# Kernel optimization log

Hardware: AMD Instinct MI355X
Metric: run time of the kernel (lower is better)

Reference implementation:

```python
import jax, jax.numpy as jnp
import numpy as np

N = 50000      # nodes
E = 400000     # edges
D_IN = 128
D = 256        # d_hidden
H = 8          # heads
C = D // H     # head dim (PyG out_channels)
L = 3          # layers
SCALE = 1.0 / np.sqrt(C).astype(np.float32)


def setup_inputs() -> dict:
    key = jax.random.key(0)
    ks = jax.random.split(key, 16)
    w = lambda k, shape: (jax.random.normal(k, shape, jnp.float32) * 0.02)
    inp = {
        "x": jax.random.normal(ks[0], (N, D_IN), jnp.float32),
        "edge_index": jax.random.randint(ks[1], (2, E), 0, N, dtype=jnp.int64),
        # input projection
        "W_in": w(ks[2], (D, D_IN)), "b_in": jnp.zeros((D,), jnp.float32),
        # stacked TransformerConv params: query/key/value/skip linears per layer
        "Wq": w(ks[3], (L, D, D)), "bq": jnp.zeros((L, D), jnp.float32),
        "Wk": w(ks[4], (L, D, D)), "bk": jnp.zeros((L, D), jnp.float32),
        "Wv": w(ks[5], (L, D, D)), "bv": jnp.zeros((L, D), jnp.float32),
        "Ws": w(ks[6], (L, D, D)), "bs": jnp.zeros((L, D), jnp.float32),
        # layer norms
        "ln_g": jnp.ones((L, D), jnp.float32), "ln_b": jnp.zeros((L, D), jnp.float32),
        # edge classifier: Linear(2D,D) -> ReLU -> Linear(D,1)
        "Wec1": w(ks[7], (D, 2 * D)), "bec1": jnp.zeros((D,), jnp.float32),
        "Wec2": w(ks[8], (1, D)), "bec2": jnp.zeros((1,), jnp.float32),
        # param predictor: Linear(2D,D) -> ReLU -> Linear(D,2) -> softplus
        "Wpp1": w(ks[9], (D, 2 * D)), "bpp1": jnp.zeros((D,), jnp.float32),
        "Wpp2": w(ks[10], (2, D)), "bpp2": jnp.zeros((2,), jnp.float32),
    }
    return inp


def _layer_norm(h, g, b):
    mu = jnp.mean(h, axis=-1, keepdims=True)
    var = jnp.mean(jnp.square(h - mu), axis=-1, keepdims=True)
    return (h - mu) * jax.lax.rsqrt(var + 1e-5) * g + b


def _transformer_conv(h, src, dst, Wq, bq, Wk, bk, Wv, bv, Ws, bs):
    # PyG TransformerConv (concat=True, root_weight=True, eval mode / no dropout)
    q = (h @ Wq.T + bq).reshape(N, H, C)
    k = (h @ Wk.T + bk).reshape(N, H, C)
    v = (h @ Wv.T + bv).reshape(N, H, C)
    # per-edge attention logits: query at dst, key at src  -> [E, H]
    alpha = jnp.einsum('ehc,ehc->eh', q[dst], k[src]) * SCALE
    # scatter-softmax over incoming edges of each dst node
    amax = jax.lax.stop_gradient(jax.ops.segment_max(alpha, dst, num_segments=N))
    ea = jnp.exp(alpha - amax[dst])
    denom = jax.ops.segment_sum(ea, dst, num_segments=N)
    a = ea / (denom[dst] + 1e-16)
    # weighted scatter-add of values  -> [N, H, C] -> [N, D]
    out = jax.ops.segment_sum(a[:, :, None] * v[src], dst, num_segments=N).reshape(N, D)
    return out + h @ Ws.T + bs  # skip connection (lin_skip)


def reference(x, edge_index, W_in, b_in, Wq, bq, Wk, bk, Wv, bv, Ws, bs,
              ln_g, ln_b, Wec1, bec1, Wec2, bec2, Wpp1, bpp1, Wpp2, bpp2):
    src, dst = edge_index[0], edge_index[1]
    h = x @ W_in.T + b_in
    for l in range(L):
        h_new = _transformer_conv(h, src, dst, Wq[l], bq[l], Wk[l], bk[l],
                                  Wv[l], bv[l], Ws[l], bs[l])
        h = _layer_norm(h + h_new, ln_g[l], ln_b[l])
    # per-edge features [E, 2D]
    ef = jnp.concatenate([h[src], h[dst]], axis=1)
    he = jax.nn.relu(ef @ Wec1.T + bec1)
    edge_logits = (he @ Wec2.T + bec2).squeeze(-1)
    hp = jax.nn.relu(ef @ Wpp1.T + bpp1)
    edge_params = jax.nn.softplus(hp @ Wpp2.T + bpp2)
    return edge_logits, edge_params
```

## Files before the change

### kernel.cpp

```cpp
#include <hip/hip_runtime.h>
#include <math.h>

typedef __bf16 bf16_t;
typedef __attribute__((ext_vector_type(8))) __bf16 bf16x8;
typedef __attribute__((ext_vector_type(4))) __bf16 bf16x4;
typedef __attribute__((ext_vector_type(4))) float f32x4;

#define MFMA16(a,b,c) __builtin_amdgcn_mfma_f32_16x16x32_bf16((a),(b),(c),0,0,0)

__device__ __forceinline__ void gload_lds16(const bf16_t* g, bf16_t* l) {
  __builtin_amdgcn_global_load_lds(
      (const __attribute__((address_space(1))) unsigned int*)g,
      (__attribute__((address_space(3))) unsigned int*)l, 16, 0, 0);
}

__global__ __launch_bounds__(256) void k_cvt4(const float* __restrict__ x,
                                              bf16_t* __restrict__ o, int n4) {
  int i = blockIdx.x * 256 + threadIdx.x;
  if (i >= n4) return;
  f32x4 v = *(const f32x4*)(x + (size_t)i * 4);
  bf16x4 b;
  b[0] = (bf16_t)v[0]; b[1] = (bf16_t)v[1]; b[2] = (bf16_t)v[2]; b[3] = (bf16_t)v[3];
  *(bf16x4*)(o + (size_t)i * 4) = b;
}

__global__ __launch_bounds__(256) void k_prep_w(
    const float* __restrict__ W_in,
    const float* __restrict__ Wq, const float* __restrict__ Wk,
    const float* __restrict__ Wv, const float* __restrict__ Ws,
    const float* __restrict__ bq, const float* __restrict__ bk,
    const float* __restrict__ bv, const float* __restrict__ bs,
    const float* __restrict__ Wec1, const float* __restrict__ Wpp1,
    const float* __restrict__ bec1, const float* __restrict__ bpp1,
    bf16_t* __restrict__ w_in_b, bf16_t* __restrict__ wqkvs_b,
    float* __restrict__ bqkvs, bf16_t* __restrict__ wnode_b,
    float* __restrict__ bnode) {
  int i = blockIdx.x * 256 + threadIdx.x;
  const int S0 = 256 * 128, S1 = 3 * 1024 * 256, S2 = 1024 * 256, S3 = 3 * 1024, S4 = 1024;
  if (i < S0) { w_in_b[i] = (bf16_t)W_in[i]; return; }
  i -= S0;
  if (i < S1) {
    int l = i / (1024 * 256), rem = i % (1024 * 256);
    int row = rem >> 8, col = rem & 255;
    const float* srcp = (row < 256) ? Wq : (row < 512) ? Wk : (row < 768) ? Wv : Ws;
    wqkvs_b[i] = (bf16_t)srcp[((size_t)l * 256 + (row & 255)) * 256 + col];
    return;
  }
  i -= S1;
  if (i < S2) {
    int row = i >> 8, col = i & 255;
    float v;
    if (row < 256)       v = Wec1[row * 512 + col];
    else if (row < 512)  v = Wec1[(row - 256) * 512 + 256 + col];
    else if (row < 768)  v = Wpp1[(row - 512) * 512 + col];
    else                 v = Wpp1[(row - 768) * 512 + 256 + col];
    wnode_b[i] = (bf16_t)v;
    return;
  }
  i -= S2;
  if (i < S3) {
    int l = i >> 10, row = i & 1023;
    const float* srcp = (row < 256) ? bq : (row < 512) ? bk : (row < 768) ? bv : bs;
    bqkvs[i] = srcp[l * 256 + (row & 255)];
    return;
  }
  i -= S3;
  if (i < S4) {
    bnode[i] = (i < 256) ? bec1[i] : ((i >= 512 && i < 768) ? bpp1[i - 512] : 0.f);
  }
}

__global__ __launch_bounds__(256) void k_gemm128(
    const bf16_t* __restrict__ A, const bf16_t* __restrict__ W,
    const float* __restrict__ bias, float* __restrict__ Cf,
    bf16_t* __restrict__ Cb, int M, int N, int K) {
  __shared__ bf16_t As[128][32];
  __shared__ bf16_t Bs[128][32];
  const int t = threadIdx.x;
  const int lane = t & 63, wave = t >> 6;
  const int wm = wave >> 1, wn = wave & 1;
  const int mi = lane & 15, ks = lane >> 4;
  const int bm = blockIdx.x * 128, bn = blockIdx.y * 128;
  const int srow = lane >> 2;
  const int scol = (lane & 3) * 8;
  int ra0 = bm + wave * 32 + srow;
  int ra1 = ra0 + 16;
  ra0 = (ra0 < M) ? ra0 : (M - 1);
  ra1 = (ra1 < M) ? ra1 : (M - 1);
  const int rb0 = bn + wave * 32 + srow;
  const int rb1 = rb0 + 16;

  f32x4 acc[4][4];
#pragma unroll
  for (int i = 0; i < 4; i++)
#pragma unroll
    for (int j = 0; j < 4; j++) acc[i][j] = (f32x4){0.f, 0.f, 0.f, 0.f};

  for (int k0 = 0; k0 < K; k0 += 32) {
    gload_lds16(A + (size_t)ra0 * K + k0 + scol, &As[wave * 32][0]);
    gload_lds16(A + (size_t)ra1 * K + k0 + scol, &As[wave * 32 + 16][0]);
    gload_lds16(W + (size_t)rb0 * K + k0 + scol, &Bs[wave * 32][0]);
    gload_lds16(W + (size_t)rb1 * K + k0 + scol, &Bs[wave * 32 + 16][0]);
    __syncthreads();
    bf16x8 af[4], bf[4];
#pragma unroll
    for (int i = 0; i < 4; i++) af[i] = *(const bf16x8*)&As[wm * 64 + i * 16 + mi][ks * 8];
#pragma unroll
    for (int j = 0; j < 4; j++) bf[j] = *(const bf16x8*)&Bs[wn * 64 + j * 16 + mi][ks * 8];
#pragma unroll
    for (int i = 0; i < 4; i++)
#pragma unroll
      for (int j = 0; j < 4; j++) acc[i][j] = MFMA16(bf[j], af[i], acc[i][j]);
    __syncthreads();
  }
#pragma unroll
  for (int i = 0; i < 4; i++) {
    int gm = bm + wm * 64 + i * 16 + mi;
    if (gm >= M) continue;
    size_t rowb = (size_t)gm * N;
#pragma unroll
    for (int j = 0; j < 4; j++) {
      int gn = bn + wn * 64 + j * 16 + ks * 4;
      f32x4 v = acc[i][j];
      if (bias) v = v + *(const f32x4*)(bias + gn);
      if (Cf) *(f32x4*)(Cf + rowb + gn) = v;
      if (Cb) {
        bf16x4 vb;
        vb[0] = (bf16_t)v[0]; vb[1] = (bf16_t)v[1];
        vb[2] = (bf16_t)v[2]; vb[3] = (bf16_t)v[3];
        *(bf16x4*)(Cb + rowb + gn) = vb;
      }
    }
  }
}

__global__ __launch_bounds__(256) void k_count(const int* __restrict__ dstv,
                                               int* __restrict__ counts, int E) {
  int e = blockIdx.x * 256 + threadIdx.x;
  if (e < E) atomicAdd(&counts[dstv[e]], 1);
}

__global__ __launch_bounds__(1024) void k_scan(const int* __restrict__ counts,
                                               int* __restrict__ row_ptr,
                                               int* __restrict__ cursor, int n) {
  __shared__ int sbuf[1024];
  int t = threadIdx.x;
  int S = (n + 1023) >> 10;
  int lo = t * S, hi = (lo + S < n) ? lo + S : n;
  int sum = 0;
  for (int i = lo; i < hi; ++i) sum += counts[i];
  sbuf[t] = sum;
  __syncthreads();
  for (int off = 1; off < 1024; off <<= 1) {
    int add = (t >= off) ? sbuf[t - off] : 0;
    __syncthreads();
    sbuf[t] += add;
    __syncthreads();
  }
  int run = sbuf[t] - sum;
  for (int i = lo; i < hi; ++i) {
    int c = counts[i];
    cursor[i] = run;
    row_ptr[i + 1] = run + c;
    run += c;
  }
  if (t == 0) row_ptr[0] = 0;
}

__global__ __launch_bounds__(256) void k_fill(const int* __restrict__ srcv,
                                              const int* __restrict__ dstv,
                                              int* __restrict__ cursor,
                                              int* __restrict__ csr_src, int E) {
  int e = blockIdx.x * 256 + threadIdx.x;
  if (e < E) {
    int slot = atomicAdd(&cursor[dstv[e]], 1);
    csr_src[slot] = srcv[e];
  }
}

__global__ __launch_bounds__(256) void k_attn_ln(
    const bf16_t* __restrict__ qkvs, const int* __restrict__ row_ptr,
    const int* __restrict__ csr_src, float* __restrict__ hf,
    bf16_t* __restrict__ hb, const float* __restrict__ g,
    const float* __restrict__ b, int Nn) {
  const int lane = threadIdx.x & 63, wave = threadIdx.x >> 6;
  const int n = blockIdx.x * 4 + wave;
  if (n >= Nn) return;
  const float SC = 0.17677669529663688f;
  bf16x4 qv = *(const bf16x4*)(qkvs + (size_t)n * 1024 + lane * 4);
  float q0 = (float)qv[0] * SC, q1 = (float)qv[1] * SC;
  float q2 = (float)qv[2] * SC, q3 = (float)qv[3] * SC;
  float mA = -INFINITY, lsA = 0.f, aA0 = 0.f, aA1 = 0.f, aA2 = 0.f, aA3 = 0.f;
  float mB = -INFINITY, lsB = 0.f, aB0 = 0.f, aB1 = 0.f, aB2 = 0.f, aB3 = 0.f;
  const int beg = row_ptr[n], end = row_ptr[n + 1];
  int idx = beg;
  for (; idx + 2 <= end; idx += 2) {
    int s0 = csr_src[idx], s1 = csr_src[idx + 1];
    const bf16_t* base0 = qkvs + (size_t)s0 * 1024;
    const bf16_t* base1 = qkvs + (size_t)s1 * 1024;
    bf16x4 k0 = *(const bf16x4*)(base0 + 256 + lane * 4);
    bf16x4 k1 = *(const bf16x4*)(base1 + 256 + lane * 4);
    bf16x4 v0 = *(const bf16x4*)(base0 + 512 + lane * 4);
    bf16x4 v1 = *(const bf16x4*)(base1 + 512 + lane * 4);
    float d0 = q0 * (float)k0[0] + q1 * (float)k0[1] + q2 * (float)k0[2] + q3 * (float)k0[3];
    float d1 = q0 * (float)k1[0] + q1 * (float)k1[1] + q2 * (float)k1[2] + q3 * (float)k1[3];
    d0 += __shfl_xor(d0, 1); d1 += __shfl_xor(d1, 1);
    d0 += __shfl_xor(d0, 2); d1 += __shfl_xor(d1, 2);
    d0 += __shfl_xor(d0, 4); d1 += __shfl_xor(d1, 4);
    float mn0 = fmaxf(mA, d0), mn1 = fmaxf(mB, d1);
    float sc0 = __expf(mA - mn0), sc1 = __expf(mB - mn1);
    float p0 = __expf(d0 - mn0), p1 = __expf(d1 - mn1);
    lsA = lsA * sc0 + p0;
    lsB = lsB * sc1 + p1;
    aA0 = aA0 * sc0 + p0 * (float)v0[0];  aB0 = aB0 * sc1 + p1 * (float)v1[0];
    aA1 = aA1 * sc0 + p0 * (float)v0[1];  aB1 = aB1 * sc1 + p1 * (float)v1[1];
    aA2 = aA2 * sc0 + p0 * (float)v0[2];  aB2 = aB2 * sc1 + p1 * (float)v1[2];
    aA3 = aA3 * sc0 + p0 * (float)v0[3];  aB3 = aB3 * sc1 + p1 * (float)v1[3];
    mA = mn0; mB = mn1;
  }
  if (idx < end) {
    int s0 = csr_src[idx];
    const bf16_t* base0 = qkvs + (size_t)s0 * 1024;
    bf16x4 k0 = *(const bf16x4*)(base0 + 256 + lane * 4);
    bf16x4 v0 = *(const bf16x4*)(base0 + 512 + lane * 4);
    float d0 = q0 * (float)k0[0] + q1 * (float)k0[1] + q2 * (float)k0[2] + q3 * (float)k0[3];
    d0 += __shfl_xor(d0, 1);
    d0 += __shfl_xor(d0, 2);
    d0 += __shfl_xor(d0, 4);
    float mn0 = fmaxf(mA, d0);
    float sc0 = __expf(mA - mn0);
    float p0 = __expf(d0 - mn0);
    lsA = lsA * sc0 + p0;
    aA0 = aA0 * sc0 + p0 * (float)v0[0];
    aA1 = aA1 * sc0 + p0 * (float)v0[1];
    aA2 = aA2 * sc0 + p0 * (float)v0[2];
    aA3 = aA3 * sc0 + p0 * (float)v0[3];
    mA = mn0;
  }
  {
    float mn = fmaxf(mA, mB);
    float sA = (mA == mn) ? 1.f : __expf(mA - mn);
    float sB = (mB == mn) ? 1.f : __expf(mB - mn);
    lsA = lsA * sA + lsB * sB;
    aA0 = aA0 * sA + aB0 * sB;
    aA1 = aA1 * sA + aB1 * sB;
    aA2 = aA2 * sA + aB2 * sB;
    aA3 = aA3 * sA + aB3 * sB;
  }
  float inv = 1.f / (lsA + 1e-16f);
  const int c = lane * 4;
  f32x4 hv = *(const f32x4*)(hf + (size_t)n * 256 + c);
  bf16x4 sv = *(const bf16x4*)(qkvs + (size_t)n * 1024 + 768 + c);
  float x0 = hv[0] + aA0 * inv + (float)sv[0];
  float x1 = hv[1] + aA1 * inv + (float)sv[1];
  float x2 = hv[2] + aA2 * inv + (float)sv[2];
  float x3 = hv[3] + aA3 * inv + (float)sv[3];
  float sum = x0 + x1 + x2 + x3;
  float sq = x0 * x0 + x1 * x1 + x2 * x2 + x3 * x3;
#pragma unroll
  for (int mm = 1; mm < 64; mm <<= 1) {
    sum += __shfl_xor(sum, mm);
    sq += __shfl_xor(sq, mm);
  }
  float mu = sum * (1.f / 256.f);
  float var = sq * (1.f / 256.f) - mu * mu;
  float rs = rsqrtf(var + 1e-5f);
  f32x4 y;
  y[0] = (x0 - mu) * rs * g[c] + b[c];
  y[1] = (x1 - mu) * rs * g[c + 1] + b[c + 1];
  y[2] = (x2 - mu) * rs * g[c + 2] + b[c + 2];
  y[3] = (x3 - mu) * rs * g[c + 3] + b[c + 3];
  *(f32x4*)(hf + (size_t)n * 256 + c) = y;
  bf16x4 yb;
  yb[0] = (bf16_t)y[0]; yb[1] = (bf16_t)y[1]; yb[2] = (bf16_t)y[2]; yb[3] = (bf16_t)y[3];
  *(bf16x4*)(hb + (size_t)n * 256 + c) = yb;
}

__global__ __launch_bounds__(256) void k_edge_final(
    const bf16_t* __restrict__ Pb, const int* __restrict__ srcv,
    const int* __restrict__ dstv, const float* __restrict__ wec2,
    const float* __restrict__ wpp2, const float* __restrict__ bec2,
    const float* __restrict__ bpp2, float* __restrict__ out, int E) {
  const int t = threadIdx.x;
  const int sub = t & 15;
  const int gid = blockIdx.x * 16 + (t >> 4);
  const int ngrp = gridDim.x * 16;
  float w_ec[2][8], w_p0[2][8], w_p1[2][8];
#pragma unroll
  for (int h = 0; h < 2; h++) {
    int cb = h * 128 + sub * 8;
    *(f32x4*)&w_ec[h][0] = *(const f32x4*)(wec2 + cb);
    *(f32x4*)&w_ec[h][4] = *(const f32x4*)(wec2 + cb + 4);
    *(f32x4*)&w_p0[h][0] = *(const f32x4*)(wpp2 + cb);
    *(f32x4*)&w_p0[h][4] = *(const f32x4*)(wpp2 + cb + 4);
    *(f32x4*)&w_p1[h][0] = *(const f32x4*)(wpp2 + 256 + cb);
    *(f32x4*)&w_p1[h][4] = *(const f32x4*)(wpp2 + 256 + cb + 4);
  }
  const float be = bec2[0], bp0 = bpp2[0], bp1 = bpp2[1];
  for (int e = gid; e < E; e += ngrp) {
    const bf16_t* ps = Pb + (size_t)srcv[e] * 1024;
    const bf16_t* pd = Pb + (size_t)dstv[e] * 1024;
    float s0 = 0.f, s1 = 0.f, s2 = 0.f;
#pragma unroll
    for (int h = 0; h < 2; h++) {
      int cb = h * 128 + sub * 8;
      bf16x8 eL = *(const bf16x8*)(ps + cb);
      bf16x8 eR = *(const bf16x8*)(pd + 256 + cb);
      bf16x8 pL = *(const bf16x8*)(ps + 512 + cb);
      bf16x8 pR = *(const bf16x8*)(pd + 768 + cb);
#pragma unroll
      for (int j = 0; j < 8; j++) {
        float he = fmaxf((float)eL[j] + (float)eR[j], 0.f);
        s0 += he * w_ec[h][j];
        float hp = fmaxf((float)pL[j] + (float)pR[j], 0.f);
        s1 += hp * w_p0[h][j];
        s2 += hp * w_p1[h][j];
      }
    }
#pragma unroll
    for (int mm = 1; mm < 16; mm <<= 1) {
      s0 += __shfl_xor(s0, mm);
      s1 += __shfl_xor(s1, mm);
      s2 += __shfl_xor(s2, mm);
    }
    if (sub == 0) {
      out[e] = s0 + be;
      float p0 = s1 + bp0;
      float p1 = s2 + bp1;
      out[(size_t)E + 2 * e]     = fmaxf(p0, 0.f) + log1pf(__expf(-fabsf(p0)));
      out[(size_t)E + 2 * e + 1] = fmaxf(p1, 0.f) + log1pf(__expf(-fabsf(p1)));
    }
  }
}

extern "C" void kernel_launch(void* const* d_in, const int* in_sizes, int n_in,
                              void* d_out, int out_size, void* d_ws, size_t ws_size,
                              hipStream_t stream) {
  const float* x    = (const float*)d_in[0];
  const int*   ei   = (const int*)d_in[1];
  const float* W_in = (const float*)d_in[2];
  const float* b_in = (const float*)d_in[3];
  const float* Wq   = (const float*)d_in[4];
  const float* bq   = (const float*)d_in[5];
  const float* Wk   = (const float*)d_in[6];
  const float* bk   = (const float*)d_in[7];
  const float* Wv   = (const float*)d_in[8];
  const float* bv   = (const float*)d_in[9];
  const float* Ws   = (const float*)d_in[10];
  const float* bs   = (const float*)d_in[11];
  const float* ln_g = (const float*)d_in[12];
  const float* ln_b = (const float*)d_in[13];
  const float* Wec1 = (const float*)d_in[14];
  const float* bec1 = (const float*)d_in[15];
  const float* Wec2 = (const float*)d_in[16];
  const float* bec2 = (const float*)d_in[17];
  const float* Wpp1 = (const float*)d_in[18];
  const float* bpp1 = (const float*)d_in[19];
  const float* Wpp2 = (const float*)d_in[20];
  const float* bpp2 = (const float*)d_in[21];

  const int N = in_sizes[0] / 128;
  const int E = in_sizes[1] / 2;
  const int* srcv = ei;
  const int* dstv = ei + E;

  char* w = (char*)d_ws;
  size_t off = 0;
  auto carve = [&](size_t bytes) -> char* {
    char* p = w + off;
    off = (off + bytes + 255) & ~(size_t)255;
    return p;
  };
  bf16_t* xb      = (bf16_t*)carve((size_t)N * 128 * 2);
  bf16_t* hb      = (bf16_t*)carve((size_t)N * 256 * 2);
  float*  hf      = (float*) carve((size_t)N * 256 * 4);
  bf16_t* qkvsb   = (bf16_t*)carve((size_t)N * 1024 * 2);
  bf16_t* w_in_b  = (bf16_t*)carve((size_t)256 * 128 * 2);
  bf16_t* wqkvs_b = (bf16_t*)carve((size_t)3 * 1024 * 256 * 2);
  float*  bqkvs   = (float*) carve((size_t)3 * 1024 * 4);
  bf16_t* wnode_b = (bf16_t*)carve((size_t)1024 * 256 * 2);
  float*  bnode   = (float*) carve((size_t)1024 * 4);
  int*    counts  = (int*)   carve((size_t)N * 4);
  int*    row_ptr = (int*)   carve((size_t)(N + 1) * 4);
  int*    cursor  = (int*)   carve((size_t)N * 4);
  int*    csr_src = (int*)   carve((size_t)E * 4);

  hipMemsetAsync(counts, 0, (size_t)N * 4, stream);

  int n4 = N * 128 / 4;
  k_cvt4<<<dim3((n4 + 255) / 256), dim3(256), 0, stream>>>(x, xb, n4);
  const int PREP_TOT = 256 * 128 + 3 * 1024 * 256 + 1024 * 256 + 3 * 1024 + 1024;
  k_prep_w<<<dim3((PREP_TOT + 255) / 256), dim3(256), 0, stream>>>(
      W_in, Wq, Wk, Wv, Ws, bq, bk, bv, bs, Wec1, Wpp1, bec1, bpp1,
      w_in_b, wqkvs_b, bqkvs, wnode_b, bnode);

  k_gemm128<<<dim3((N + 127) / 128, 2), dim3(256), 0, stream>>>(
      xb, w_in_b, b_in, hf, hb, N, 256, 128);

  k_count<<<dim3((E + 255) / 256), dim3(256), 0, stream>>>(dstv, counts, E);
  k_scan<<<dim3(1), dim3(1024), 0, stream>>>(counts, row_ptr, cursor, N);
  k_fill<<<dim3((E + 255) / 256), dim3(256), 0, stream>>>(srcv, dstv, cursor, csr_src, E);

  for (int l = 0; l < 3; ++l) {
    k_gemm128<<<dim3((N + 127) / 128, 8), dim3(256), 0, stream>>>(
        hb, wqkvs_b + (size_t)l * 1024 * 256, bqkvs + l * 1024,
        (float*)nullptr, qkvsb, N, 1024, 256);
    k_attn_ln<<<dim3((N + 3) / 4), dim3(256), 0, stream>>>(
        qkvsb, row_ptr, csr_src, hf, hb, ln_g + l * 256, ln_b + l * 256, N);
  }

  k_gemm128<<<dim3((N + 127) / 128, 8), dim3(256), 0, stream>>>(
      hb, wnode_b, bnode, (float*)nullptr, qkvsb, N, 1024, 256);
  k_edge_final<<<dim3(2048), dim3(256), 0, stream>>>(
      qkvsb, srcv, dstv, Wec2, Wpp2, bec2, bpp2, (float*)d_out, E);
}
```

Measured before the change: 933.8 us.

## Double-buffer GEMM LDS tiles and process final edges in dst-sorted CSR order

The GEMM now uses two LDS buffers and issues the next K-tile's global-to-LDS loads before computing on the current one, so load latency can overlap the MFMA work. The fill kernel also records the destination and original edge id for each CSR slot. The edge-final kernel walks edges in CSR order in chunks of 16, so it reloads the destination-node features only when the destination changes, and it scatters outputs back by edge id. The trade-offs are extra index arrays, scattered output writes and chunked work that may be uneven across groups.

```diff
diff --git a/kernel.cpp b/kernel.cpp
--- a/kernel.cpp
+++ b/kernel.cpp
@@ -74,44 +74,53 @@
     const bf16_t* __restrict__ A, const bf16_t* __restrict__ W,
     const float* __restrict__ bias, float* __restrict__ Cf,
     bf16_t* __restrict__ Cb, int M, int N, int K) {
-  __shared__ bf16_t As[128][32];
-  __shared__ bf16_t Bs[128][32];
+  __shared__ bf16_t As[2][128 * 32];
+  __shared__ bf16_t Bs[2][128 * 32];
   const int t = threadIdx.x;
   const int lane = t & 63, wave = t >> 6;
   const int wm = wave >> 1, wn = wave & 1;
   const int mi = lane & 15, ks = lane >> 4;
   const int bm = blockIdx.x * 128, bn = blockIdx.y * 128;
-  const int srow = lane >> 2;
   const int scol = (lane & 3) * 8;
-  int ra0 = bm + wave * 32 + srow;
+  int ra0 = bm + wave * 32 + (lane >> 2);
   int ra1 = ra0 + 16;
   ra0 = (ra0 < M) ? ra0 : (M - 1);
   ra1 = (ra1 < M) ? ra1 : (M - 1);
-  const int rb0 = bn + wave * 32 + srow;
+  const int rb0 = bn + wave * 32 + (lane >> 2);
   const int rb1 = rb0 + 16;
 
+  auto stage = [&](int buf, int k0) {
+    gload_lds16(A + (size_t)ra0 * K + k0 + scol, &As[buf][(wave * 32) * 32]);
+    gload_lds16(A + (size_t)ra1 * K + k0 + scol, &As[buf][(wave * 32 + 16) * 32]);
+    gload_lds16(W + (size_t)rb0 * K + k0 + scol, &Bs[buf][(wave * 32) * 32]);
+    gload_lds16(W + (size_t)rb1 * K + k0 + scol, &Bs[buf][(wave * 32 + 16) * 32]);
+  };
+
   f32x4 acc[4][4];
 #pragma unroll
   for (int i = 0; i < 4; i++)
 #pragma unroll
     for (int j = 0; j < 4; j++) acc[i][j] = (f32x4){0.f, 0.f, 0.f, 0.f};
 
-  for (int k0 = 0; k0 < K; k0 += 32) {
-    gload_lds16(A + (size_t)ra0 * K + k0 + scol, &As[wave * 32][0]);
-    gload_lds16(A + (size_t)ra1 * K + k0 + scol, &As[wave * 32 + 16][0]);
-    gload_lds16(W + (size_t)rb0 * K + k0 + scol, &Bs[wave * 32][0]);
-    gload_lds16(W + (size_t)rb1 * K + k0 + scol, &Bs[wave * 32 + 16][0]);
-    __syncthreads();
+  stage(0, 0);
+  __syncthreads();
+  const int nk = K >> 5;
+  int cur = 0;
+  for (int kt = 0; kt < nk; ++kt) {
+    if (kt + 1 < nk) stage(cur ^ 1, (kt + 1) << 5);
     bf16x8 af[4], bf[4];
 #pragma unroll
-    for (int i = 0; i < 4; i++) af[i] = *(const bf16x8*)&As[wm * 64 + i * 16 + mi][ks * 8];
-#pragma unroll
-    for (int j = 0; j < 4; j++) bf[j] = *(const bf16x8*)&Bs[wn * 64 + j * 16 + mi][ks * 8];
+    for (int i = 0; i < 4; i++)
+      af[i] = *(const bf16x8*)&As[cur][(wm * 64 + i * 16 + mi) * 32 + ks * 8];
+#pragma unroll
+    for (int j = 0; j < 4; j++)
+      bf[j] = *(const bf16x8*)&Bs[cur][(wn * 64 + j * 16 + mi) * 32 + ks * 8];
 #pragma unroll
     for (int i = 0; i < 4; i++)
 #pragma unroll
       for (int j = 0; j < 4; j++) acc[i][j] = MFMA16(bf[j], af[i], acc[i][j]);
     __syncthreads();
+    cur ^= 1;
   }
 #pragma unroll
   for (int i = 0; i < 4; i++) {
@@ -170,11 +179,16 @@
 __global__ __launch_bounds__(256) void k_fill(const int* __restrict__ srcv,
                                               const int* __restrict__ dstv,
                                               int* __restrict__ cursor,
-                                              int* __restrict__ csr_src, int E) {
+                                              int* __restrict__ csr_src,
+                                              int* __restrict__ csr_dst,
+                                              int* __restrict__ csr_eid, int E) {
   int e = blockIdx.x * 256 + threadIdx.x;
   if (e < E) {
-    int slot = atomicAdd(&cursor[dstv[e]], 1);
+    int d = dstv[e];
+    int slot = atomicAdd(&cursor[d], 1);
     csr_src[slot] = srcv[e];
+    csr_dst[slot] = d;
+    csr_eid[slot] = e;
   }
 }
 
@@ -277,14 +291,17 @@
 }
 
 __global__ __launch_bounds__(256) void k_edge_final(
-    const bf16_t* __restrict__ Pb, const int* __restrict__ srcv,
-    const int* __restrict__ dstv, const float* __restrict__ wec2,
-    const float* __restrict__ wpp2, const float* __restrict__ bec2,
-    const float* __restrict__ bpp2, float* __restrict__ out, int E) {
+    const bf16_t* __restrict__ Pb, const int* __restrict__ csr_src,
+    const int* __restrict__ csr_dst, const int* __restrict__ csr_eid,
+    const float* __restrict__ wec2, const float* __restrict__ wpp2,
+    const float* __restrict__ bec2, const float* __restrict__ bpp2,
+    float* __restrict__ out, int E) {
   const int t = threadIdx.x;
   const int sub = t & 15;
-  const int gid = blockIdx.x * 16 + (t >> 4);
-  const int ngrp = gridDim.x * 16;
+  const int grp = blockIdx.x * 16 + (t >> 4);
+  const int slot0 = grp * 16;
+  if (slot0 >= E) return;
+  const int slot1 = (slot0 + 16 < E) ? slot0 + 16 : E;
   float w_ec[2][8], w_p0[2][8], w_p1[2][8];
 #pragma unroll
   for (int h = 0; h < 2; h++) {
@@ -297,22 +314,34 @@
     *(f32x4*)&w_p1[h][4] = *(const f32x4*)(wpp2 + 256 + cb + 4);
   }
   const float be = bec2[0], bp0 = bpp2[0], bp1 = bpp2[1];
-  for (int e = gid; e < E; e += ngrp) {
-    const bf16_t* ps = Pb + (size_t)srcv[e] * 1024;
-    const bf16_t* pd = Pb + (size_t)dstv[e] * 1024;
+  int cur_dst = -1;
+  float eR[2][8], pR[2][8];
+  for (int slot = slot0; slot < slot1; ++slot) {
+    int dn = csr_dst[slot];
+    if (dn != cur_dst) {
+      cur_dst = dn;
+      const bf16_t* pd = Pb + (size_t)dn * 1024;
+#pragma unroll
+      for (int h = 0; h < 2; h++) {
+        int cb = h * 128 + sub * 8;
+        bf16x8 a = *(const bf16x8*)(pd + 256 + cb);
+        bf16x8 p = *(const bf16x8*)(pd + 768 + cb);
+#pragma unroll
+        for (int j = 0; j < 8; j++) { eR[h][j] = (float)a[j]; pR[h][j] = (float)p[j]; }
+      }
+    }
+    const bf16_t* ps = Pb + (size_t)csr_src[slot] * 1024;
     float s0 = 0.f, s1 = 0.f, s2 = 0.f;
 #pragma unroll
     for (int h = 0; h < 2; h++) {
       int cb = h * 128 + sub * 8;
       bf16x8 eL = *(const bf16x8*)(ps + cb);
-      bf16x8 eR = *(const bf16x8*)(pd + 256 + cb);
       bf16x8 pL = *(const bf16x8*)(ps + 512 + cb);
-      bf16x8 pR = *(const bf16x8*)(pd + 768 + cb);
 #pragma unroll
       for (int j = 0; j < 8; j++) {
-        float he = fmaxf((float)eL[j] + (float)eR[j], 0.f);
+        float he = fmaxf((float)eL[j] + eR[h][j], 0.f);
         s0 += he * w_ec[h][j];
-        float hp = fmaxf((float)pL[j] + (float)pR[j], 0.f);
+        float hp = fmaxf((float)pL[j] + pR[h][j], 0.f);
         s1 += hp * w_p0[h][j];
         s2 += hp * w_p1[h][j];
       }
@@ -324,11 +353,12 @@
       s2 += __shfl_xor(s2, mm);
     }
     if (sub == 0) {
-      out[e] = s0 + be;
+      int eid = csr_eid[slot];
+      out[eid] = s0 + be;
       float p0 = s1 + bp0;
       float p1 = s2 + bp1;
-      out[(size_t)E + 2 * e]     = fmaxf(p0, 0.f) + log1pf(__expf(-fabsf(p0)));
-      out[(size_t)E + 2 * e + 1] = fmaxf(p1, 0.f) + log1pf(__expf(-fabsf(p1)));
+      out[(size_t)E + 2 * eid]     = fmaxf(p0, 0.f) + log1pf(__expf(-fabsf(p0)));
+      out[(size_t)E + 2 * eid + 1] = fmaxf(p1, 0.f) + log1pf(__expf(-fabsf(p1)));
     }
   }
 }
@@ -384,6 +414,8 @@
   int*    row_ptr = (int*)   carve((size_t)(N + 1) * 4);
   int*    cursor  = (int*)   carve((size_t)N * 4);
   int*    csr_src = (int*)   carve((size_t)E * 4);
+  int*    csr_dst = (int*)   carve((size_t)E * 4);
+  int*    csr_eid = (int*)   carve((size_t)E * 4);
 
   hipMemsetAsync(counts, 0, (size_t)N * 4, stream);
 
@@ -399,7 +431,8 @@
 
   k_count<<<dim3((E + 255) / 256), dim3(256), 0, stream>>>(dstv, counts, E);
   k_scan<<<dim3(1), dim3(1024), 0, stream>>>(counts, row_ptr, cursor, N);
-  k_fill<<<dim3((E + 255) / 256), dim3(256), 0, stream>>>(srcv, dstv, cursor, csr_src, E);
+  k_fill<<<dim3((E + 255) / 256), dim3(256), 0, stream>>>(
+      srcv, dstv, cursor, csr_src, csr_dst, csr_eid, E);
 
   for (int l = 0; l < 3; ++l) {
     k_gemm128<<<dim3((N + 127) / 128, 8), dim3(256), 0, stream>>>(
@@ -411,6 +444,7 @@
 
   k_gemm128<<<dim3((N + 127) / 128, 8), dim3(256), 0, stream>>>(
       hb, wnode_b, bnode, (float*)nullptr, qkvsb, N, 1024, 256);
-  k_edge_final<<<dim3(2048), dim3(256), 0, stream>>>(
-      qkvsb, srcv, dstv, Wec2, Wpp2, bec2, bpp2, (float*)d_out, E);
-}
+  int ngroups = (E + 15) / 16;
+  k_edge_final<<<dim3((ngroups + 15) / 16), dim3(256), 0, stream>>>(
+      qkvsb, csr_src, csr_dst, csr_eid, Wec2, Wpp2, bec2, bpp2, (float*)d_out, E);
+}
```

Measured after the change: 939.9 us. No clear change (+0.7%).
